# Kernel optimization log

Hardware: AMD Instinct MI355X
Metric: run time of the kernel (lower is better)

The kernel has to match this reference:

```python
import jax, jax.numpy as jnp
import numpy as np

# dims matching init_kwargs / input_specs
B, N, HID = 1, 200000, 256
NH, S = 8, 64
DH = HID // NH  # 32
STD = 0.02


def setup_inputs() -> dict:
    key = jax.random.key(0)
    ks = jax.random.split(key, 12)
    x = jax.random.normal(ks[0], (B, N, HID), jnp.float32)
    attn_mask = jnp.ones((B, N), jnp.float32)
    # Linear weights stored as (in, out); torch uses y = x @ W.T + b but init is random so layout is a convention.
    W_fx = jax.random.normal(ks[1], (HID, HID), jnp.float32) * STD
    b_fx = jnp.zeros((HID,), jnp.float32)
    W_x = jax.random.normal(ks[2], (HID, HID), jnp.float32) * STD
    b_x = jnp.zeros((HID,), jnp.float32)
    W_slice = jax.random.normal(ks[3], (DH, S), jnp.float32) * STD
    b_slice = jnp.zeros((S,), jnp.float32)
    W_qkv = jax.random.normal(ks[4], (DH, 3 * DH), jnp.float32) * STD  # bias=False
    W_proj = jax.random.normal(ks[5], (HID, HID), jnp.float32) * STD
    b_proj = jnp.zeros((HID,), jnp.float32)
    temperature = jnp.full((1, NH, 1, 1), 0.5, jnp.float32)
    return dict(x=x, attn_mask=attn_mask, W_fx=W_fx, b_fx=b_fx, W_x=W_x, b_x=b_x,
                W_slice=W_slice, b_slice=b_slice, W_qkv=W_qkv,
                W_proj=W_proj, b_proj=b_proj, temperature=temperature)


def reference(x, attn_mask, W_fx, b_fx, W_x, b_x, W_slice, b_slice, W_qkv, W_proj, b_proj, temperature):
    b, n, hid = x.shape
    # project and split heads: [b, h, n, c]
    fx_mid = (x @ W_fx + b_fx).reshape(b, n, NH, DH).transpose(0, 2, 1, 3)
    x_mid = (x @ W_x + b_x).reshape(b, n, NH, DH).transpose(0, 2, 1, 3)
    # slice logits [b, h, n, s], temperature-scaled softmax over slices
    slice_logits = (x_mid @ W_slice + b_slice) / temperature
    slice_weights = jax.nn.softmax(slice_logits, axis=-1)
    slice_weights = slice_weights * attn_mask[:, None, :, None]
    slice_norm = slice_weights.sum(axis=2)[..., None]  # [b, h, s, 1]
    # weighted-pool tokens into slice tokens [b, h, s, c]
    slice_tokens = jnp.einsum('bhnc,bhns->bhsc', fx_mid, slice_weights) / (slice_norm + 1e-5)
    # SDPA over the small slice axis
    q, k, v = jnp.split(slice_tokens @ W_qkv, 3, axis=-1)
    scale = 1.0 / np.sqrt(DH).astype(np.float32)
    attn = jax.nn.softmax(jnp.einsum('bhsc,bhtc->bhst', q, k) * scale, axis=-1)
    out_slice = jnp.einsum('bhst,bhtc->bhsc', attn, v)
    # scatter back to tokens [b, h, n, c] -> [b, n, hid]
    out_x = jnp.einsum('bhsc,bhns->bhnc', out_slice, slice_weights)
    out_x = out_x.transpose(0, 2, 1, 3).reshape(b, n, hid)
    out_x = out_x * attn_mask[..., None]
    out = out_x @ W_proj + b_proj
    return out * attn_mask[..., None]
```

## Files before the change

### kernel.cpp

```cpp
#include <hip/hip_runtime.h>


#define HID 256
#define NH  8
#define DH  32
#define NS  64
#define NQ  512
#define TT  64
#define PSTRIDE 16896

typedef short bf16x8 __attribute__((ext_vector_type(8)));
typedef short bf16x4 __attribute__((ext_vector_type(4)));
typedef float f32x4 __attribute__((ext_vector_type(4)));

#define MFMA(a,b,c) __builtin_amdgcn_mfma_f32_16x16x32_bf16((a),(b),(c),0,0,0)

__device__ __forceinline__ f32x4 mfma16(bf16x4 a, bf16x4 b, f32x4 c) {
#if __has_builtin(__builtin_amdgcn_mfma_f32_16x16x16bf16_1k)
  return __builtin_amdgcn_mfma_f32_16x16x16bf16_1k(a, b, c, 0, 0, 0);
#elif __has_builtin(__builtin_amdgcn_mfma_f32_16x16x16_bf16)
  return __builtin_amdgcn_mfma_f32_16x16x16_bf16(a, b, c, 0, 0, 0);
#else
  f32x4 d;
  asm("v_mfma_f32_16x16x16_bf16 %0, %1, %2, %3" : "=v"(d) : "v"(a), "v"(b), "v"(c));
  return d;
#endif
}

__device__ __forceinline__ f32x4 zero4() { f32x4 z; z[0]=0.f; z[1]=0.f; z[2]=0.f; z[3]=0.f; return z; }

__device__ __forceinline__ ushort bf_rne(float f) {
  unsigned u = __float_as_uint(f);
  return (ushort)((u + 0x7FFFu + ((u >> 16) & 1u)) >> 16);
}
__device__ __forceinline__ void split2(float f, ushort& h, ushort& l) {
  h = bf_rne(f);
  float fh = __uint_as_float(((unsigned)h) << 16);
  l = bf_rne(f - fh);
}
__device__ __forceinline__ uint pack2(float f) {
  ushort h, l; split2(f, h, l);
  return ((uint)h << 16) | (uint)l;
}
__device__ __forceinline__ bf16x4 pack4(float a0, float a1, float a2, float a3) {
  union { ushort u[4]; bf16x4 v; } P;
  P.u[0] = bf_rne(a0); P.u[1] = bf_rne(a1); P.u[2] = bf_rne(a2); P.u[3] = bf_rne(a3);
  return P.v;
}

__global__ __launch_bounds__(256) void k_build_wlog(
    const float* __restrict__ Wx, const float* __restrict__ bx,
    const float* __restrict__ Wsl, const float* __restrict__ bsl,
    const float* __restrict__ temp,
    ushort* __restrict__ wlh, ushort* __restrict__ wll, float* __restrict__ blog)
{
  const int q = blockIdx.x, k = threadIdx.x;
  const int h = q >> 6, s = q & 63;
  const float it = 1.0f / temp[h];
  float acc = 0.f;
#pragma unroll
  for (int c = 0; c < DH; ++c)
    acc = fmaf(Wx[k * HID + h * DH + c], Wsl[c * NS + s], acc);
  acc *= it;
  ushort hh, ll; split2(acc, hh, ll);
  wlh[q * HID + k] = hh; wll[q * HID + k] = ll;
  if (k == 0) {
    float b = bsl[s];
    for (int c = 0; c < DH; ++c) b = fmaf(bx[h * DH + c], Wsl[c * NS + s], b);
    blog[q] = b * it;
  }
}

__global__ __launch_bounds__(256) void k_build_wfxt(
    const float* __restrict__ Wfx, ushort* __restrict__ wfxth)
{
  const int c = blockIdx.x, k = threadIdx.x;
  wfxth[c * HID + k] = bf_rne(Wfx[k * HID + c]);
}

__global__ __launch_bounds__(256) void k_build_wprojt(
    const float* __restrict__ Wproj, ushort* __restrict__ wpth, ushort* __restrict__ wptl)
{
  const int hc = blockIdx.x, j = threadIdx.x;
  ushort hh, ll; split2(Wproj[hc * HID + j], hh, ll);
  wpth[j * HID + hc] = hh; wptl[j * HID + hc] = ll;
}

__global__ __launch_bounds__(512, 1) void k_pass1T2(
    const float* __restrict__ x, const float* __restrict__ mask,
    const ushort* __restrict__ wlogh, const float* __restrict__ blog,
    const ushort* __restrict__ wfxth, const float* __restrict__ bfx,
    float* __restrict__ partials, int Ntok, int ntiles, int ngrid)
{
  __shared__ ushort xh[TT * 264];
  __shared__ float msk[TT];

  const int t = threadIdx.x;
  const int wv = t >> 6, lane = t & 63, lr = lane & 15, lg = lane >> 4;
  const int h = wv;

  float blogr[4], bfxr[2];
#pragma unroll
  for (int cf = 0; cf < 4; ++cf) blogr[cf] = blog[h * 64 + cf * 16 + lr];
#pragma unroll
  for (int cf2 = 0; cf2 < 2; ++cf2) bfxr[cf2] = bfx[h * 32 + cf2 * 16 + lr];

  f32x4 pool[4][2];
#pragma unroll
  for (int cf = 0; cf < 4; ++cf) { pool[cf][0] = zero4(); pool[cf][1] = zero4(); }
  float nacc[4] = {0.f, 0.f, 0.f, 0.f};

  for (int tile = blockIdx.x; tile < ntiles; tile += ngrid) {
    const int n0 = tile * TT;
    __syncthreads();
    {
      const int tok = t >> 3, seg = (t & 7) * 32;
      const int n = n0 + tok;
      const float* xrow = x + (size_t)n * HID + seg;
#pragma unroll
      for (int g = 0; g < 4; ++g) {
        float v[8];
        if (n < Ntok) {
          const float4* xp = (const float4*)(xrow + g * 8);
          float4 f0 = xp[0], f1 = xp[1];
          v[0]=f0.x; v[1]=f0.y; v[2]=f0.z; v[3]=f0.w;
          v[4]=f1.x; v[5]=f1.y; v[6]=f1.z; v[7]=f1.w;
        } else {
#pragma unroll
          for (int i = 0; i < 8; ++i) v[i] = 0.f;
        }
        union { ushort u[8]; bf16x8 v8; } H;
#pragma unroll
        for (int i = 0; i < 8; ++i) H.u[i] = bf_rne(v[i]);
        *reinterpret_cast<bf16x8*>(&xh[tok * 264 + seg + g * 8]) = H.v8;
      }
      if (t < TT) msk[t] = (n0 + t < Ntok) ? mask[n0 + t] : 0.f;
    }
    __syncthreads();

    f32x4 acc[4][4];
#pragma unroll
    for (int rf = 0; rf < 4; ++rf)
#pragma unroll
      for (int cf = 0; cf < 4; ++cf) acc[rf][cf] = zero4();
#pragma unroll
    for (int kk = 0; kk < 8; ++kk) {
      bf16x8 a[4];
#pragma unroll
      for (int rf = 0; rf < 4; ++rf)
        a[rf] = *reinterpret_cast<const bf16x8*>(&xh[(rf * 16 + lr) * 264 + kk * 32 + lg * 8]);
#pragma unroll
      for (int cf = 0; cf < 4; ++cf) {
        bf16x8 bh = *reinterpret_cast<const bf16x8*>(wlogh + (size_t)(h * 64 + cf * 16 + lr) * HID + kk * 32 + lg * 8);
#pragma unroll
        for (int rf = 0; rf < 4; ++rf) acc[rf][cf] = MFMA(a[rf], bh, acc[rf][cf]);
      }
    }
    bf16x4 aw[4][4];
#pragma unroll
    for (int rf = 0; rf < 4; ++rf) {
#pragma unroll
      for (int r = 0; r < 4; ++r) {
        float mx = -1e30f;
#pragma unroll
        for (int cf = 0; cf < 4; ++cf) { float vv = acc[rf][cf][r] + blogr[cf]; acc[rf][cf][r] = vv; mx = fmaxf(mx, vv); }
        mx = fmaxf(mx, __shfl_xor(mx, 1)); mx = fmaxf(mx, __shfl_xor(mx, 2));
        mx = fmaxf(mx, __shfl_xor(mx, 4)); mx = fmaxf(mx, __shfl_xor(mx, 8));
        float sm = 0.f;
#pragma unroll
        for (int cf = 0; cf < 4; ++cf) { float e = __expf(acc[rf][cf][r] - mx); acc[rf][cf][r] = e; sm += e; }
        sm += __shfl_xor(sm, 1); sm += __shfl_xor(sm, 2); sm += __shfl_xor(sm, 4); sm += __shfl_xor(sm, 8);
        const float sc = msk[rf * 16 + lg * 4 + r] / sm;
#pragma unroll
        for (int cf = 0; cf < 4; ++cf) { acc[rf][cf][r] *= sc; nacc[cf] += acc[rf][cf][r]; }
      }
#pragma unroll
      for (int cf = 0; cf < 4; ++cf)
        aw[rf][cf] = pack4(acc[rf][cf][0], acc[rf][cf][1], acc[rf][cf][2], acc[rf][cf][3]);
    }
    f32x4 fa[4][2];
#pragma unroll
    for (int rf = 0; rf < 4; ++rf) { fa[rf][0] = zero4(); fa[rf][1] = zero4(); }
#pragma unroll
    for (int kk = 0; kk < 8; ++kk) {
      bf16x8 a[4];
#pragma unroll
      for (int rf = 0; rf < 4; ++rf)
        a[rf] = *reinterpret_cast<const bf16x8*>(&xh[(rf * 16 + lr) * 264 + kk * 32 + lg * 8]);
#pragma unroll
      for (int cf2 = 0; cf2 < 2; ++cf2) {
        bf16x8 bf = *reinterpret_cast<const bf16x8*>(wfxth + (size_t)(h * 32 + cf2 * 16 + lr) * HID + kk * 32 + lg * 8);
#pragma unroll
        for (int rf = 0; rf < 4; ++rf) fa[rf][cf2] = MFMA(a[rf], bf, fa[rf][cf2]);
      }
    }
#pragma unroll
    for (int rf = 0; rf < 4; ++rf) {
      bf16x4 bfrag[2];
#pragma unroll
      for (int cf2 = 0; cf2 < 2; ++cf2)
        bfrag[cf2] = pack4(fa[rf][cf2][0] + bfxr[cf2], fa[rf][cf2][1] + bfxr[cf2],
                           fa[rf][cf2][2] + bfxr[cf2], fa[rf][cf2][3] + bfxr[cf2]);
#pragma unroll
      for (int cf = 0; cf < 4; ++cf)
#pragma unroll
        for (int cf2 = 0; cf2 < 2; ++cf2)
          pool[cf][cf2] = mfma16(aw[rf][cf], bfrag[cf2], pool[cf][cf2]);
    }
  }
  float* pb = partials + (size_t)blockIdx.x * PSTRIDE;
#pragma unroll
  for (int cf = 0; cf < 4; ++cf)
#pragma unroll
    for (int cf2 = 0; cf2 < 2; ++cf2)
#pragma unroll
      for (int r = 0; r < 4; ++r) {
        const int s = cf * 16 + lg * 4 + r;
        const int hcl = cf2 * 16 + lr;
        pb[h * 2048 + s * 32 + hcl] = pool[cf][cf2][r];
      }
#pragma unroll
  for (int cf = 0; cf < 4; ++cf) {
    float v = nacc[cf];
    v += __shfl_xor(v, 16); v += __shfl_xor(v, 32);
    if (lg == 0) pb[16384 + h * 64 + cf * 16 + lr] = v;
  }
}

__global__ __launch_bounds__(256) void k_reduce_norm(
    const float* __restrict__ partials, float* __restrict__ normbuf, int nb)
{
  const int p = blockIdx.x * 256 + threadIdx.x;
  float s = 0.f;
  for (int b = 0; b < nb; ++b) s += partials[(size_t)b * PSTRIDE + 16384 + p];
  normbuf[p] = s;
}

__global__ __launch_bounds__(256) void k_reduce_num(
    const float* __restrict__ partials, const float* __restrict__ normbuf,
    float* __restrict__ st, int nb)
{
  const int pidx = blockIdx.x * 256 + threadIdx.x;
  float acc = 0.f;
  for (int b = 0; b < nb; ++b) acc += partials[(size_t)b * PSTRIDE + pidx];
  st[pidx] = acc / (normbuf[pidx >> 5] + 1e-5f);
}

__global__ __launch_bounds__(64) void k_sdpa(
    const float* __restrict__ st, const float* __restrict__ Wqkv,
    uint* __restrict__ osltp)
{
  __shared__ float stt[NS][DH + 1];
  __shared__ float kt[NS][DH + 1];
  __shared__ float vt[NS][DH + 1];
  const int h = blockIdx.x, sr = threadIdx.x;
  for (int i = sr; i < NS * DH; i += 64) stt[i >> 5][i & 31] = st[(size_t)h * NS * DH + i];
  __syncthreads();
  float qr[DH];
#pragma unroll
  for (int c = 0; c < DH; ++c) {
    float aq = 0.f, ak = 0.f, av = 0.f;
#pragma unroll
    for (int i = 0; i < DH; ++i) {
      const float sv = stt[sr][i];
      aq = fmaf(sv, Wqkv[i * 96 + c], aq);
      ak = fmaf(sv, Wqkv[i * 96 + 32 + c], ak);
      av = fmaf(sv, Wqkv[i * 96 + 64 + c], av);
    }
    qr[c] = aq; kt[sr][c] = ak; vt[sr][c] = av;
  }
  __syncthreads();
  float sc[NS];
  float m = -1e30f;
  const float scale = 0.17677669529663687f;
#pragma unroll
  for (int tt = 0; tt < NS; ++tt) {
    float a = 0.f;
#pragma unroll
    for (int c = 0; c < DH; ++c) a = fmaf(qr[c], kt[tt][c], a);
    a *= scale; sc[tt] = a; m = fmaxf(m, a);
  }
  float sum = 0.f;
#pragma unroll
  for (int tt = 0; tt < NS; ++tt) { const float e = __expf(sc[tt] - m); sc[tt] = e; sum += e; }
  const float inv = 1.f / sum;
#pragma unroll
  for (int c = 0; c < DH; ++c) {
    float o = 0.f;
#pragma unroll
    for (int tt = 0; tt < NS; ++tt) o = fmaf(sc[tt], vt[tt][c], o);
    o *= inv;
    osltp[(h * DH + c) * NS + sr] = pack2(o);
  }
}

__global__ __launch_bounds__(512, 2) void k_pass3T(
    const float* __restrict__ x, const float* __restrict__ mask,
    const ushort* __restrict__ wlogh, const ushort* __restrict__ wlogl,
    const float* __restrict__ blog,
    const uint* __restrict__ osltp,
    const ushort* __restrict__ wpth, const ushort* __restrict__ wptl,
    const float* __restrict__ bproj,
    float* __restrict__ out, int Ntok, int ntiles, int ngrid)
{
  __shared__ uint smem[TT * 268];
  __shared__ float msk[TT];
  ushort* xh = (ushort*)smem;
  ushort* xl = xh + TT * 264;
  uint*   ox32 = smem;
  float*  outs = (float*)smem;

  const int t = threadIdx.x;
  const int wv = t >> 6, lane = t & 63, lr = lane & 15, lg = lane >> 4;
  const int h = wv;

  float bprr[2];
#pragma unroll
  for (int cf = 0; cf < 2; ++cf) bprr[cf] = bproj[wv * 32 + cf * 16 + lr];
  float4 blgv[4];
#pragma unroll
  for (int cf = 0; cf < 4; ++cf)
    blgv[cf] = *reinterpret_cast<const float4*>(blog + h * 64 + cf * 16 + lg * 4);

  bf16x4 oslh[2][4], osll[2][4];
#pragma unroll
  for (int cfo = 0; cfo < 2; ++cfo)
#pragma unroll
    for (int sb = 0; sb < 4; ++sb) {
      const uint4 q = *reinterpret_cast<const uint4*>(
          osltp + (size_t)(h * DH + cfo * 16 + lr) * NS + sb * 16 + lg * 4);
      union { uint u[2]; bf16x4 v; } Hc, Lc;
      Hc.u[0] = __builtin_amdgcn_perm(q.y, q.x, 0x07060302u);
      Hc.u[1] = __builtin_amdgcn_perm(q.w, q.z, 0x07060302u);
      Lc.u[0] = __builtin_amdgcn_perm(q.y, q.x, 0x05040100u);
      Lc.u[1] = __builtin_amdgcn_perm(q.w, q.z, 0x05040100u);
      oslh[cfo][sb] = Hc.v; osll[cfo][sb] = Lc.v;
    }

  for (int tile = blockIdx.x; tile < ntiles; tile += ngrid) {
    const int n0 = tile * TT;
    __syncthreads();
    {
      const int tok = t >> 3, seg = (t & 7) * 32;
      const int n = n0 + tok;
      const float* xrow = x + (size_t)n * HID + seg;
#pragma unroll
      for (int g = 0; g < 4; ++g) {
        float v[8];
        if (n < Ntok) {
          const float4* xp = (const float4*)(xrow + g * 8);
          float4 f0 = xp[0], f1 = xp[1];
          v[0]=f0.x; v[1]=f0.y; v[2]=f0.z; v[3]=f0.w;
          v[4]=f1.x; v[5]=f1.y; v[6]=f1.z; v[7]=f1.w;
        } else {
#pragma unroll
          for (int i = 0; i < 8; ++i) v[i] = 0.f;
        }
        union { ushort u[8]; bf16x8 v8; } H, L;
#pragma unroll
        for (int i = 0; i < 8; ++i) split2(v[i], H.u[i], L.u[i]);
        *reinterpret_cast<bf16x8*>(&xh[tok * 264 + seg + g * 8]) = H.v8;
        *reinterpret_cast<bf16x8*>(&xl[tok * 264 + seg + g * 8]) = L.v8;
      }
      if (t < TT) msk[t] = (n0 + t < Ntok) ? mask[n0 + t] : 0.f;
    }
    __syncthreads();

    f32x4 acc[4][4];
#pragma unroll
    for (int rf = 0; rf < 4; ++rf)
#pragma unroll
      for (int cf = 0; cf < 4; ++cf) acc[rf][cf] = zero4();
#pragma unroll
    for (int kk = 0; kk < 8; ++kk) {
      bf16x8 bx_h[4], bx_l[4];
#pragma unroll
      for (int rf = 0; rf < 4; ++rf) {
        bx_h[rf] = *reinterpret_cast<const bf16x8*>(&xh[(rf * 16 + lr) * 264 + kk * 32 + lg * 8]);
        bx_l[rf] = *reinterpret_cast<const bf16x8*>(&xl[(rf * 16 + lr) * 264 + kk * 32 + lg * 8]);
      }
#pragma unroll
      for (int cf = 0; cf < 4; ++cf) {
        const size_t bo = (size_t)(h * 64 + cf * 16 + lr) * HID + kk * 32 + lg * 8;
        bf16x8 ah = *reinterpret_cast<const bf16x8*>(wlogh + bo);
        bf16x8 al = *reinterpret_cast<const bf16x8*>(wlogl + bo);
#pragma unroll
        for (int rf = 0; rf < 4; ++rf) {
          acc[rf][cf] = MFMA(ah, bx_h[rf], acc[rf][cf]);
          acc[rf][cf] = MFMA(al, bx_h[rf], acc[rf][cf]);
          acc[rf][cf] = MFMA(ah, bx_l[rf], acc[rf][cf]);
        }
      }
    }
#pragma unroll
    for (int rf = 0; rf < 4; ++rf) {
      float mx = -1e30f;
#pragma unroll
      for (int cf = 0; cf < 4; ++cf)
#pragma unroll
        for (int r = 0; r < 4; ++r) {
          float vv = acc[rf][cf][r] + ((const float*)&blgv[cf])[r];
          acc[rf][cf][r] = vv; mx = fmaxf(mx, vv);
        }
      mx = fmaxf(mx, __shfl_xor(mx, 16)); mx = fmaxf(mx, __shfl_xor(mx, 32));
      float sm = 0.f;
#pragma unroll
      for (int cf = 0; cf < 4; ++cf)
#pragma unroll
        for (int r = 0; r < 4; ++r) { float e = __expf(acc[rf][cf][r] - mx); acc[rf][cf][r] = e; sm += e; }
      sm += __shfl_xor(sm, 16); sm += __shfl_xor(sm, 32);
      const float sc = msk[rf * 16 + lr] / sm;
#pragma unroll
      for (int cf = 0; cf < 4; ++cf)
#pragma unroll
        for (int r = 0; r < 4; ++r) acc[rf][cf][r] *= sc;
    }
    f32x4 oxacc[4][2];
#pragma unroll
    for (int rf = 0; rf < 4; ++rf) { oxacc[rf][0] = zero4(); oxacc[rf][1] = zero4(); }
#pragma unroll
    for (int rf = 0; rf < 4; ++rf) {
      uint w32[4][4];
#pragma unroll
      for (int cf = 0; cf < 4; ++cf)
#pragma unroll
        for (int r = 0; r < 4; ++r) w32[cf][r] = pack2(acc[rf][cf][r]);
#pragma unroll
      for (int sb = 0; sb < 4; ++sb) {
        union { uint u[2]; bf16x4 v; } Hc, Lc;
        Hc.u[0] = __builtin_amdgcn_perm(w32[sb][1], w32[sb][0], 0x07060302u);
        Hc.u[1] = __builtin_amdgcn_perm(w32[sb][3], w32[sb][2], 0x07060302u);
        Lc.u[0] = __builtin_amdgcn_perm(w32[sb][1], w32[sb][0], 0x05040100u);
        Lc.u[1] = __builtin_amdgcn_perm(w32[sb][3], w32[sb][2], 0x05040100u);
#pragma unroll
        for (int cfo = 0; cfo < 2; ++cfo) {
          oxacc[rf][cfo] = mfma16(Hc.v, oslh[cfo][sb], oxacc[rf][cfo]);
          oxacc[rf][cfo] = mfma16(Lc.v, oslh[cfo][sb], oxacc[rf][cfo]);
          oxacc[rf][cfo] = mfma16(Hc.v, osll[cfo][sb], oxacc[rf][cfo]);
        }
      }
    }
    __syncthreads();
#pragma unroll
    for (int rf = 0; rf < 4; ++rf)
#pragma unroll
      for (int cfo = 0; cfo < 2; ++cfo)
#pragma unroll
        for (int r = 0; r < 4; ++r) {
          const int tok = rf * 16 + lg * 4 + r;
          const int hc = h * DH + cfo * 16 + lr;
          ox32[tok * 268 + hc] = pack2(oxacc[rf][cfo][r]);
        }
    __syncthreads();
    f32x4 s2[4][2];
#pragma unroll
    for (int rf = 0; rf < 4; ++rf) { s2[rf][0] = zero4(); s2[rf][1] = zero4(); }
#pragma unroll
    for (int kk = 0; kk < 8; ++kk) {
#pragma unroll
      for (int rf = 0; rf < 4; ++rf) {
        const uint* oxp = &ox32[(rf * 16 + lr) * 268 + kk * 32 + lg * 8];
        uint4 q0 = *reinterpret_cast<const uint4*>(oxp);
        uint4 q1 = *reinterpret_cast<const uint4*>(oxp + 4);
        union { uint u[4]; bf16x8 v; } AH, AL;
        AH.u[0] = __builtin_amdgcn_perm(q0.y, q0.x, 0x07060302u);
        AH.u[1] = __builtin_amdgcn_perm(q0.w, q0.z, 0x07060302u);
        AH.u[2] = __builtin_amdgcn_perm(q1.y, q1.x, 0x07060302u);
        AH.u[3] = __builtin_amdgcn_perm(q1.w, q1.z, 0x07060302u);
        AL.u[0] = __builtin_amdgcn_perm(q0.y, q0.x, 0x05040100u);
        AL.u[1] = __builtin_amdgcn_perm(q0.w, q0.z, 0x05040100u);
        AL.u[2] = __builtin_amdgcn_perm(q1.y, q1.x, 0x05040100u);
        AL.u[3] = __builtin_amdgcn_perm(q1.w, q1.z, 0x05040100u);
#pragma unroll
        for (int cf = 0; cf < 2; ++cf) {
          const size_t bo = (size_t)(wv * 32 + cf * 16 + lr) * HID + kk * 32 + lg * 8;
          bf16x8 bh = *reinterpret_cast<const bf16x8*>(wpth + bo);
          bf16x8 bl = *reinterpret_cast<const bf16x8*>(wptl + bo);
          s2[rf][cf] = MFMA(AH.v, bh, s2[rf][cf]);
          s2[rf][cf] = MFMA(AL.v, bh, s2[rf][cf]);
          s2[rf][cf] = MFMA(AH.v, bl, s2[rf][cf]);
        }
      }
    }
    __syncthreads();
#pragma unroll
    for (int rf = 0; rf < 4; ++rf)
#pragma unroll
      for (int cf = 0; cf < 2; ++cf)
#pragma unroll
        for (int r = 0; r < 4; ++r) {
          const int tok = rf * 16 + lg * 4 + r;
          const int j = wv * 32 + cf * 16 + lr;
          const float mk = msk[tok];
          outs[tok * 268 + j] = mk * (mk * s2[rf][cf][r] + bprr[cf]);
        }
    __syncthreads();
    {
      const int tok0 = t >> 8, col = t & 255;
#pragma unroll 4
      for (int rr = 0; rr < TT / 2; ++rr) {
        const int tok = rr * 2 + tok0;
        const int n = n0 + tok;
        if (n < Ntok)
          __builtin_nontemporal_store(outs[tok * 268 + col],
                                      &out[(size_t)n * HID + col]);
      }
    }
  }
}

extern "C" void kernel_launch(void* const* d_in, const int* in_sizes, int n_in,
                              void* d_out, int out_size, void* d_ws, size_t ws_size,
                              hipStream_t stream)
{
  const float* x     = (const float*)d_in[0];
  const float* mask  = (const float*)d_in[1];
  const float* Wfx   = (const float*)d_in[2];
  const float* bfx   = (const float*)d_in[3];
  const float* Wx    = (const float*)d_in[4];
  const float* bx    = (const float*)d_in[5];
  const float* Wsl   = (const float*)d_in[6];
  const float* bsl   = (const float*)d_in[7];
  const float* Wqkv  = (const float*)d_in[8];
  const float* Wproj = (const float*)d_in[9];
  const float* bproj = (const float*)d_in[10];
  const float* temp  = (const float*)d_in[11];
  float* out = (float*)d_out;

  const int Ntok = in_sizes[0] / HID;
  const int ntiles = (Ntok + TT - 1) / TT;

  char* ws = (char*)d_ws;
  size_t off = 0;
  ushort* wlogh = (ushort*)(ws + off); off += (size_t)NQ * HID * 2;
  ushort* wlogl = (ushort*)(ws + off); off += (size_t)NQ * HID * 2;
  float*  blog  = (float*)(ws + off);  off += NQ * 4;
  ushort* wfxth = (ushort*)(ws + off); off += (size_t)HID * HID * 2;
  ushort* wpth  = (ushort*)(ws + off); off += (size_t)HID * HID * 2;
  ushort* wptl  = (ushort*)(ws + off); off += (size_t)HID * HID * 2;
  uint*   osltp = (uint*)(ws + off);   off += (size_t)NQ * DH * 4;
  float*  stb   = (float*)(ws + off);  off += (size_t)NQ * DH * 4;
  float*  normb = (float*)(ws + off);  off += NQ * 4;
  int nbp = 512;
  while (nbp > 1 && off + (size_t)nbp * PSTRIDE * 4 > ws_size) nbp >>= 1;
  float* partials = (float*)(ws + off);

  k_build_wlog<<<dim3(NQ), dim3(256), 0, stream>>>(Wx, bx, Wsl, bsl, temp, wlogh, wlogl, blog);
  k_build_wfxt<<<dim3(HID), dim3(256), 0, stream>>>(Wfx, wfxth);
  k_build_wprojt<<<dim3(HID), dim3(256), 0, stream>>>(Wproj, wpth, wptl);
  k_pass1T2<<<dim3(nbp), dim3(512), 0, stream>>>(x, mask, wlogh, blog, wfxth, bfx,
                                                 partials, Ntok, ntiles, nbp);
  k_reduce_norm<<<dim3(2), dim3(256), 0, stream>>>(partials, normb, nbp);
  k_reduce_num<<<dim3(64), dim3(256), 0, stream>>>(partials, normb, stb, nbp);
  k_sdpa<<<dim3(NH), dim3(64), 0, stream>>>(stb, Wqkv, osltp);
  k_pass3T<<<dim3(256), dim3(512), 0, stream>>>(x, mask, wlogh, wlogl, blog,
                                                osltp, wpth, wptl, bproj,
                                                out, Ntok, ntiles, 256);
}
```

Before: 1.119 ms.

## Materialize slice weights in pass1 and reuse them in pass3

Pass 1 now computes the slice logits with split high/low bf16 precision, applies the masked softmax, and writes the per-token slice weights to a workspace buffer as packed hi/lo bf16 pairs. A new pass 3 reads those weights instead of reloading x and recomputing the logit GEMM and softmax. This removes the duplicated logit computation in the scatter pass. In exchange it writes and later reads a weight buffer about twice the size of x, and it only runs when the workspace is large enough; otherwise the old path is used.

Result: slower. 1.370 ms (+22.5%).

```diff
diff --git a/kernel.cpp b/kernel.cpp
--- a/kernel.cpp
+++ b/kernel.cpp
@@ -86,13 +86,16 @@
   wpth[j * HID + hc] = hh; wptl[j * HID + hc] = ll;
 }
 
-__global__ __launch_bounds__(512, 1) void k_pass1T2(
+__global__ __launch_bounds__(512, 1) void k_pass1W(
     const float* __restrict__ x, const float* __restrict__ mask,
-    const ushort* __restrict__ wlogh, const float* __restrict__ blog,
+    const ushort* __restrict__ wlogh, const ushort* __restrict__ wlogl,
+    const float* __restrict__ blog,
     const ushort* __restrict__ wfxth, const float* __restrict__ bfx,
+    uint* __restrict__ w32g,
     float* __restrict__ partials, int Ntok, int ntiles, int ngrid)
 {
   __shared__ ushort xh[TT * 264];
+  __shared__ ushort xl[TT * 264];
   __shared__ float msk[TT];
 
   const int t = threadIdx.x;
@@ -129,6 +132,163 @@
 #pragma unroll
           for (int i = 0; i < 8; ++i) v[i] = 0.f;
         }
+        union { ushort u[8]; bf16x8 v8; } H, L;
+#pragma unroll
+        for (int i = 0; i < 8; ++i) split2(v[i], H.u[i], L.u[i]);
+        *reinterpret_cast<bf16x8*>(&xh[tok * 264 + seg + g * 8]) = H.v8;
+        *reinterpret_cast<bf16x8*>(&xl[tok * 264 + seg + g * 8]) = L.v8;
+      }
+      if (t < TT) msk[t] = (n0 + t < Ntok) ? mask[n0 + t] : 0.f;
+    }
+    __syncthreads();
+
+    f32x4 acc[4][4];
+#pragma unroll
+    for (int rf = 0; rf < 4; ++rf)
+#pragma unroll
+      for (int cf = 0; cf < 4; ++cf) acc[rf][cf] = zero4();
+#pragma unroll
+    for (int kk = 0; kk < 8; ++kk) {
+      bf16x8 ah[4], al_[4];
+#pragma unroll
+      for (int rf = 0; rf < 4; ++rf) {
+        ah[rf]  = *reinterpret_cast<const bf16x8*>(&xh[(rf * 16 + lr) * 264 + kk * 32 + lg * 8]);
+        al_[rf] = *reinterpret_cast<const bf16x8*>(&xl[(rf * 16 + lr) * 264 + kk * 32 + lg * 8]);
+      }
+#pragma unroll
+      for (int cf = 0; cf < 4; ++cf) {
+        const size_t bo = (size_t)(h * 64 + cf * 16 + lr) * HID + kk * 32 + lg * 8;
+        bf16x8 bh = *reinterpret_cast<const bf16x8*>(wlogh + bo);
+        bf16x8 bl = *reinterpret_cast<const bf16x8*>(wlogl + bo);
+#pragma unroll
+        for (int rf = 0; rf < 4; ++rf) {
+          acc[rf][cf] = MFMA(ah[rf], bh, acc[rf][cf]);
+          acc[rf][cf] = MFMA(al_[rf], bh, acc[rf][cf]);
+          acc[rf][cf] = MFMA(ah[rf], bl, acc[rf][cf]);
+        }
+      }
+    }
+    bf16x4 aw[4][4];
+#pragma unroll
+    for (int rf = 0; rf < 4; ++rf) {
+#pragma unroll
+      for (int r = 0; r < 4; ++r) {
+        float mx = -1e30f;
+#pragma unroll
+        for (int cf = 0; cf < 4; ++cf) { float vv = acc[rf][cf][r] + blogr[cf]; acc[rf][cf][r] = vv; mx = fmaxf(mx, vv); }
+        mx = fmaxf(mx, __shfl_xor(mx, 1)); mx = fmaxf(mx, __shfl_xor(mx, 2));
+        mx = fmaxf(mx, __shfl_xor(mx, 4)); mx = fmaxf(mx, __shfl_xor(mx, 8));
+        float sm = 0.f;
+#pragma unroll
+        for (int cf = 0; cf < 4; ++cf) { float e = __expf(acc[rf][cf][r] - mx); acc[rf][cf][r] = e; sm += e; }
+        sm += __shfl_xor(sm, 1); sm += __shfl_xor(sm, 2); sm += __shfl_xor(sm, 4); sm += __shfl_xor(sm, 8);
+        const float sc = msk[rf * 16 + lg * 4 + r] / sm;
+        const int n = n0 + rf * 16 + lg * 4 + r;
+#pragma unroll
+        for (int cf = 0; cf < 4; ++cf) {
+          acc[rf][cf][r] *= sc;
+          nacc[cf] += acc[rf][cf][r];
+          if (n < Ntok)
+            __builtin_nontemporal_store(pack2(acc[rf][cf][r]),
+                &w32g[(size_t)n * NQ + h * 64 + cf * 16 + lr]);
+        }
+      }
+#pragma unroll
+      for (int cf = 0; cf < 4; ++cf)
+        aw[rf][cf] = pack4(acc[rf][cf][0], acc[rf][cf][1], acc[rf][cf][2], acc[rf][cf][3]);
+    }
+    f32x4 fa[4][2];
+#pragma unroll
+    for (int rf = 0; rf < 4; ++rf) { fa[rf][0] = zero4(); fa[rf][1] = zero4(); }
+#pragma unroll
+    for (int kk = 0; kk < 8; ++kk) {
+      bf16x8 a[4];
+#pragma unroll
+      for (int rf = 0; rf < 4; ++rf)
+        a[rf] = *reinterpret_cast<const bf16x8*>(&xh[(rf * 16 + lr) * 264 + kk * 32 + lg * 8]);
+#pragma unroll
+      for (int cf2 = 0; cf2 < 2; ++cf2) {
+        bf16x8 bf = *reinterpret_cast<const bf16x8*>(wfxth + (size_t)(h * 32 + cf2 * 16 + lr) * HID + kk * 32 + lg * 8);
+#pragma unroll
+        for (int rf = 0; rf < 4; ++rf) fa[rf][cf2] = MFMA(a[rf], bf, fa[rf][cf2]);
+      }
+    }
+#pragma unroll
+    for (int rf = 0; rf < 4; ++rf) {
+      bf16x4 bfrag[2];
+#pragma unroll
+      for (int cf2 = 0; cf2 < 2; ++cf2)
+        bfrag[cf2] = pack4(fa[rf][cf2][0] + bfxr[cf2], fa[rf][cf2][1] + bfxr[cf2],
+                           fa[rf][cf2][2] + bfxr[cf2], fa[rf][cf2][3] + bfxr[cf2]);
+#pragma unroll
+      for (int cf = 0; cf < 4; ++cf)
+#pragma unroll
+        for (int cf2 = 0; cf2 < 2; ++cf2)
+          pool[cf][cf2] = mfma16(aw[rf][cf], bfrag[cf2], pool[cf][cf2]);
+    }
+  }
+  float* pb = partials + (size_t)blockIdx.x * PSTRIDE;
+#pragma unroll
+  for (int cf = 0; cf < 4; ++cf)
+#pragma unroll
+    for (int cf2 = 0; cf2 < 2; ++cf2)
+#pragma unroll
+      for (int r = 0; r < 4; ++r) {
+        const int s = cf * 16 + lg * 4 + r;
+        const int hcl = cf2 * 16 + lr;
+        pb[h * 2048 + s * 32 + hcl] = pool[cf][cf2][r];
+      }
+#pragma unroll
+  for (int cf = 0; cf < 4; ++cf) {
+    float v = nacc[cf];
+    v += __shfl_xor(v, 16); v += __shfl_xor(v, 32);
+    if (lg == 0) pb[16384 + h * 64 + cf * 16 + lr] = v;
+  }
+}
+
+__global__ __launch_bounds__(512, 1) void k_pass1T2(
+    const float* __restrict__ x, const float* __restrict__ mask,
+    const ushort* __restrict__ wlogh, const float* __restrict__ blog,
+    const ushort* __restrict__ wfxth, const float* __restrict__ bfx,
+    float* __restrict__ partials, int Ntok, int ntiles, int ngrid)
+{
+  __shared__ ushort xh[TT * 264];
+  __shared__ float msk[TT];
+
+  const int t = threadIdx.x;
+  const int wv = t >> 6, lane = t & 63, lr = lane & 15, lg = lane >> 4;
+  const int h = wv;
+
+  float blogr[4], bfxr[2];
+#pragma unroll
+  for (int cf = 0; cf < 4; ++cf) blogr[cf] = blog[h * 64 + cf * 16 + lr];
+#pragma unroll
+  for (int cf2 = 0; cf2 < 2; ++cf2) bfxr[cf2] = bfx[h * 32 + cf2 * 16 + lr];
+
+  f32x4 pool[4][2];
+#pragma unroll
+  for (int cf = 0; cf < 4; ++cf) { pool[cf][0] = zero4(); pool[cf][1] = zero4(); }
+  float nacc[4] = {0.f, 0.f, 0.f, 0.f};
+
+  for (int tile = blockIdx.x; tile < ntiles; tile += ngrid) {
+    const int n0 = tile * TT;
+    __syncthreads();
+    {
+      const int tok = t >> 3, seg = (t & 7) * 32;
+      const int n = n0 + tok;
+      const float* xrow = x + (size_t)n * HID + seg;
+#pragma unroll
+      for (int g = 0; g < 4; ++g) {
+        float v[8];
+        if (n < Ntok) {
+          const float4* xp = (const float4*)(xrow + g * 8);
+          float4 f0 = xp[0], f1 = xp[1];
+          v[0]=f0.x; v[1]=f0.y; v[2]=f0.z; v[3]=f0.w;
+          v[4]=f1.x; v[5]=f1.y; v[6]=f1.z; v[7]=f1.w;
+        } else {
+#pragma unroll
+          for (int i = 0; i < 8; ++i) v[i] = 0.f;
+        }
         union { ushort u[8]; bf16x8 v8; } H;
 #pragma unroll
         for (int i = 0; i < 8; ++i) H.u[i] = bf_rne(v[i]);
@@ -291,6 +451,141 @@
     for (int tt = 0; tt < NS; ++tt) o = fmaf(sc[tt], vt[tt][c], o);
     o *= inv;
     osltp[(h * DH + c) * NS + sr] = pack2(o);
+  }
+}
+
+__global__ __launch_bounds__(512, 2) void k_pass3W(
+    const float* __restrict__ mask,
+    const uint* __restrict__ w32g,
+    const uint* __restrict__ osltp,
+    const ushort* __restrict__ wpth, const ushort* __restrict__ wptl,
+    const float* __restrict__ bproj,
+    float* __restrict__ out, int Ntok, int ntiles, int ngrid)
+{
+  __shared__ uint ox32[TT * 268];
+  __shared__ float msk[TT];
+  float* outs = (float*)ox32;
+
+  const int t = threadIdx.x;
+  const int wv = t >> 6, lane = t & 63, lr = lane & 15, lg = lane >> 4;
+  const int h = wv;
+
+  float bprr[2];
+#pragma unroll
+  for (int cf = 0; cf < 2; ++cf) bprr[cf] = bproj[wv * 32 + cf * 16 + lr];
+
+  bf16x4 oslh[2][4], osll[2][4];
+#pragma unroll
+  for (int cfo = 0; cfo < 2; ++cfo)
+#pragma unroll
+    for (int sb = 0; sb < 4; ++sb) {
+      const uint4 q = *reinterpret_cast<const uint4*>(
+          osltp + (size_t)(h * DH + cfo * 16 + lr) * NS + sb * 16 + lg * 4);
+      union { uint u[2]; bf16x4 v; } Hc, Lc;
+      Hc.u[0] = __builtin_amdgcn_perm(q.y, q.x, 0x07060302u);
+      Hc.u[1] = __builtin_amdgcn_perm(q.w, q.z, 0x07060302u);
+      Lc.u[0] = __builtin_amdgcn_perm(q.y, q.x, 0x05040100u);
+      Lc.u[1] = __builtin_amdgcn_perm(q.w, q.z, 0x05040100u);
+      oslh[cfo][sb] = Hc.v; osll[cfo][sb] = Lc.v;
+    }
+
+  const uint4 zq = {0u, 0u, 0u, 0u};
+
+  for (int tile = blockIdx.x; tile < ntiles; tile += ngrid) {
+    const int n0 = tile * TT;
+    if (t < TT) msk[t] = (n0 + t < Ntok) ? mask[n0 + t] : 0.f;
+
+    f32x4 oxacc[4][2];
+#pragma unroll
+    for (int rf = 0; rf < 4; ++rf) { oxacc[rf][0] = zero4(); oxacc[rf][1] = zero4(); }
+#pragma unroll
+    for (int rf = 0; rf < 4; ++rf) {
+      const int n = n0 + rf * 16 + lr;
+#pragma unroll
+      for (int sb = 0; sb < 4; ++sb) {
+        uint4 q = zq;
+        if (n < Ntok)
+          q = *reinterpret_cast<const uint4*>(
+              w32g + (size_t)n * NQ + h * 64 + sb * 16 + lg * 4);
+        union { uint u[2]; bf16x4 v; } Hc, Lc;
+        Hc.u[0] = __builtin_amdgcn_perm(q.y, q.x, 0x07060302u);
+        Hc.u[1] = __builtin_amdgcn_perm(q.w, q.z, 0x07060302u);
+        Lc.u[0] = __builtin_amdgcn_perm(q.y, q.x, 0x05040100u);
+        Lc.u[1] = __builtin_amdgcn_perm(q.w, q.z, 0x05040100u);
+#pragma unroll
+        for (int cfo = 0; cfo < 2; ++cfo) {
+          oxacc[rf][cfo] = mfma16(Hc.v, oslh[cfo][sb], oxacc[rf][cfo]);
+          oxacc[rf][cfo] = mfma16(Lc.v, oslh[cfo][sb], oxacc[rf][cfo]);
+          oxacc[rf][cfo] = mfma16(Hc.v, osll[cfo][sb], oxacc[rf][cfo]);
+        }
+      }
+    }
+    __syncthreads();
+#pragma unroll
+    for (int rf = 0; rf < 4; ++rf)
+#pragma unroll
+      for (int cfo = 0; cfo < 2; ++cfo)
+#pragma unroll
+        for (int r = 0; r < 4; ++r) {
+          const int tok = rf * 16 + lg * 4 + r;
+          const int hc = h * DH + cfo * 16 + lr;
+          ox32[tok * 268 + hc] = pack2(oxacc[rf][cfo][r]);
+        }
+    __syncthreads();
+    f32x4 s2[4][2];
+#pragma unroll
+    for (int rf = 0; rf < 4; ++rf) { s2[rf][0] = zero4(); s2[rf][1] = zero4(); }
+#pragma unroll
+    for (int kk = 0; kk < 8; ++kk) {
+#pragma unroll
+      for (int rf = 0; rf < 4; ++rf) {
+        const uint* oxp = &ox32[(rf * 16 + lr) * 268 + kk * 32 + lg * 8];
+        uint4 q0 = *reinterpret_cast<const uint4*>(oxp);
+        uint4 q1 = *reinterpret_cast<const uint4*>(oxp + 4);
+        union { uint u[4]; bf16x8 v; } AH, AL;
+        AH.u[0] = __builtin_amdgcn_perm(q0.y, q0.x, 0x07060302u);
+        AH.u[1] = __builtin_amdgcn_perm(q0.w, q0.z, 0x07060302u);
+        AH.u[2] = __builtin_amdgcn_perm(q1.y, q1.x, 0x07060302u);
+        AH.u[3] = __builtin_amdgcn_perm(q1.w, q1.z, 0x07060302u);
+        AL.u[0] = __builtin_amdgcn_perm(q0.y, q0.x, 0x05040100u);
+        AL.u[1] = __builtin_amdgcn_perm(q0.w, q0.z, 0x05040100u);
+        AL.u[2] = __builtin_amdgcn_perm(q1.y, q1.x, 0x05040100u);
+        AL.u[3] = __builtin_amdgcn_perm(q1.w, q1.z, 0x05040100u);
+#pragma unroll
+        for (int cf = 0; cf < 2; ++cf) {
+          const size_t bo = (size_t)(wv * 32 + cf * 16 + lr) * HID + kk * 32 + lg * 8;
+          bf16x8 bh = *reinterpret_cast<const bf16x8*>(wpth + bo);
+          bf16x8 bl = *reinterpret_cast<const bf16x8*>(wptl + bo);
+          s2[rf][cf] = MFMA(AH.v, bh, s2[rf][cf]);
+          s2[rf][cf] = MFMA(AL.v, bh, s2[rf][cf]);
+          s2[rf][cf] = MFMA(AH.v, bl, s2[rf][cf]);
+        }
+      }
+    }
+    __syncthreads();
+#pragma unroll
+    for (int rf = 0; rf < 4; ++rf)
+#pragma unroll
+      for (int cf = 0; cf < 2; ++cf)
+#pragma unroll
+        for (int r = 0; r < 4; ++r) {
+          const int tok = rf * 16 + lg * 4 + r;
+          const int j = wv * 32 + cf * 16 + lr;
+          const float mk = msk[tok];
+          outs[tok * 268 + j] = mk * (mk * s2[rf][cf][r] + bprr[cf]);
+        }
+    __syncthreads();
+    {
+      const int tok0 = t >> 8, col = t & 255;
+#pragma unroll 4
+      for (int rr = 0; rr < TT / 2; ++rr) {
+        const int tok = rr * 2 + tok0;
+        const int n = n0 + tok;
+        if (n < Ntok)
+          __builtin_nontemporal_store(outs[tok * 268 + col],
+                                      &out[(size_t)n * HID + col]);
+      }
+    }
   }
 }
 
@@ -544,16 +839,31 @@
   int nbp = 512;
   while (nbp > 1 && off + (size_t)nbp * PSTRIDE * 4 > ws_size) nbp >>= 1;
   float* partials = (float*)(ws + off);
+  const size_t off_p = off + (size_t)nbp * PSTRIDE * 4;
+  const size_t needW = off_p + (size_t)Ntok * NQ * 4 + 256;
 
   k_build_wlog<<<dim3(NQ), dim3(256), 0, stream>>>(Wx, bx, Wsl, bsl, temp, wlogh, wlogl, blog);
   k_build_wfxt<<<dim3(HID), dim3(256), 0, stream>>>(Wfx, wfxth);
   k_build_wprojt<<<dim3(HID), dim3(256), 0, stream>>>(Wproj, wpth, wptl);
-  k_pass1T2<<<dim3(nbp), dim3(512), 0, stream>>>(x, mask, wlogh, blog, wfxth, bfx,
-                                                 partials, Ntok, ntiles, nbp);
-  k_reduce_norm<<<dim3(2), dim3(256), 0, stream>>>(partials, normb, nbp);
-  k_reduce_num<<<dim3(64), dim3(256), 0, stream>>>(partials, normb, stb, nbp);
-  k_sdpa<<<dim3(NH), dim3(64), 0, stream>>>(stb, Wqkv, osltp);
-  k_pass3T<<<dim3(256), dim3(512), 0, stream>>>(x, mask, wlogh, wlogl, blog,
-                                                osltp, wpth, wptl, bproj,
-                                                out, Ntok, ntiles, 256);
-}
+
+  if (ws_size >= needW) {
+    uint* w32g = (uint*)(ws + off_p);
+    k_pass1W<<<dim3(nbp), dim3(512), 0, stream>>>(x, mask, wlogh, wlogl, blog,
+                                                  wfxth, bfx, w32g,
+                                                  partials, Ntok, ntiles, nbp);
+    k_reduce_norm<<<dim3(2), dim3(256), 0, stream>>>(partials, normb, nbp);
+    k_reduce_num<<<dim3(64), dim3(256), 0, stream>>>(partials, normb, stb, nbp);
+    k_sdpa<<<dim3(NH), dim3(64), 0, stream>>>(stb, Wqkv, osltp);
+    k_pass3W<<<dim3(512), dim3(512), 0, stream>>>(mask, w32g, osltp, wpth, wptl,
+                                                  bproj, out, Ntok, ntiles, 512);
+  } else {
+    k_pass1T2<<<dim3(nbp), dim3(512), 0, stream>>>(x, mask, wlogh, blog, wfxth, bfx,
+                                                   partials, Ntok, ntiles, nbp);
+    k_reduce_norm<<<dim3(2), dim3(256), 0, stream>>>(partials, normb, nbp);
+    k_reduce_num<<<dim3(64), dim3(256), 0, stream>>>(partials, normb, stb, nbp);
+    k_sdpa<<<dim3(NH), dim3(64), 0, stream>>>(stb, Wqkv, osltp);
+    k_pass3T<<<dim3(256), dim3(512), 0, stream>>>(x, mask, wlogh, wlogl, blog,
+                                                  osltp, wpth, wptl, bproj,
+                                                  out, Ntok, ntiles, 256);
+  }
+}
```
